# Kernel tuning notes

Hardware: AMD Instinct MI355X
Metric: run time of the kernel (lower is better)

Reference implementation:

```python
import jax, jax.numpy as jnp
import numpy as np

NB_CLUSTERS = 128   # C: number of clusters (equal-size, sorted ids)
PTS_PER_CLUSTER = 1024  # P: points per cluster
DIM = 3


def setup_inputs() -> dict:
    key = jax.random.key(0)
    k1, k2 = jax.random.split(key)
    n = NB_CLUSTERS * PTS_PER_CLUSTER
    input_points = jax.random.normal(k1, (n, DIM), dtype=jnp.float32)
    output_points = jax.random.normal(k2, (n, DIM), dtype=jnp.float32)
    clusters = jnp.repeat(jnp.arange(NB_CLUSTERS, dtype=jnp.int32), PTS_PER_CLUSTER)
    return {
        "input_points": input_points,
        "input_clusters": clusters,
        "output_points": output_points,
        "output_clusters": clusters,
    }


def reference(input_points, input_clusters, output_points, output_clusters):
    # Original: nb_clusters = max(input_clusters); loop for i in range(nb_clusters)
    # -> the HIGHEST cluster id is excluded from the loss. Reproduced via mask.
    nb = jnp.max(input_clusters)  # == NB_CLUSTERS - 1
    a = input_points.reshape(NB_CLUSTERS, PTS_PER_CLUSTER, DIM)   # [C,P,3]
    b = output_points.reshape(NB_CLUSTERS, PTS_PER_CLUSTER, DIM)  # [C,P,3]

    # Pairwise squared distances per cluster: d[c,i,j] = ||a[c,i]-b[c,j]||^2
    d = (jnp.sum(a * a, axis=-1)[:, :, None]
         + jnp.sum(b * b, axis=-1)[:, None, :]
         - 2.0 * jnp.einsum('cid,cjd->cij', a, b))  # [C,P,P]

    # Indices computed under no_grad in the original (ints: no grad anyway).
    idx1 = jnp.argmin(d, axis=2)  # for each input point: nearest output point
    idx2 = jnp.argmin(d, axis=1)  # for each output point: nearest input point

    near_b = jnp.take_along_axis(b, idx1[..., None], axis=1)  # [C,P,3]
    near_a = jnp.take_along_axis(a, idx2[..., None], axis=1)  # [C,P,3]

    l1 = jnp.sum((a - near_b) ** 2, axis=(1, 2))  # [C]
    l2 = jnp.sum((b - near_a) ** 2, axis=(1, 2))  # [C]

    mask = (jnp.arange(NB_CLUSTERS) < nb).astype(a.dtype)  # exclude last cluster
    return jnp.sum(mask * (l1 + l2))
```

## Files before the change

### kernel.cpp

```cpp
#include <hip/hip_runtime.h>


#define PTS  1024
#define ACTIVE_CLUSTERS 127
#define QG   64
#define Q    16
#define SEG  16
#define TPB  1024
#define TSEG (PTS / SEG)

typedef float v2f __attribute__((ext_vector_type(2)));

static __device__ __forceinline__ v2f splat2(float a) {
    v2f r; r.x = a; r.y = a; return r;
}

__global__
__attribute__((amdgpu_flat_work_group_size(TPB, TPB), amdgpu_waves_per_eu(4, 4)))
void chamfer_kernel(
    const float* __restrict__ pts_in,
    const float* __restrict__ pts_out,
    float* __restrict__ out)
{
    const int c   = blockIdx.x >> 1;
    const int dir = blockIdx.x & 1;

    const float* __restrict__ query  = dir ? pts_out : pts_in;
    const float* __restrict__ target = dir ? pts_in  : pts_out;

    __shared__ __align__(16) float sx[PTS];
    __shared__ __align__(16) float sy[PTS];
    __shared__ __align__(16) float sz[PTS];
    __shared__ __align__(16) float sh[PTS];
    __shared__ unsigned colmin[PTS];
    __shared__ float wsum[16];

    const int tid = threadIdx.x;
    const int qi  = tid & (QG - 1);
    const int seg = tid >> 6;
    const size_t base = (size_t)c * PTS * 3;

    colmin[tid] = 0x7f7fffffu;

    {
        const float* tp = target + base + (size_t)tid * 3;
        float x = tp[0], y = tp[1], z = tp[2];
        sx[tid] = x; sy[tid] = y; sz[tid] = z;
        sh[tid] = fmaf(x, x, fmaf(y, y, z * z));
    }

    float qx[Q], qy[Q], qz[Q], mn[Q];
    #pragma unroll
    for (int k = 0; k < Q; ++k) {
        const float* qp = query + base + (size_t)(k * QG + qi) * 3;
        qx[k] = -2.0f * qp[0];
        qy[k] = -2.0f * qp[1];
        qz[k] = -2.0f * qp[2];
        mn[k] = 3.4e38f;
    }
    __syncthreads();

    const int j0 = seg * TSEG;
    #pragma unroll 1
    for (int jj = 0; jj < TSEG; jj += 4) {
        const float4 bx = *(const float4*)&sx[j0 + jj];
        const float4 by = *(const float4*)&sy[j0 + jj];
        const float4 bz = *(const float4*)&sz[j0 + jj];
        const float4 bh = *(const float4*)&sh[j0 + jj];
        v2f bx01; bx01.x = bx.x; bx01.y = bx.y;
        v2f bx23; bx23.x = bx.z; bx23.y = bx.w;
        v2f by01; by01.x = by.x; by01.y = by.y;
        v2f by23; by23.x = by.z; by23.y = by.w;
        v2f bz01; bz01.x = bz.x; bz01.y = bz.y;
        v2f bz23; bz23.x = bz.z; bz23.y = bz.w;
        v2f bh01; bh01.x = bh.x; bh01.y = bh.y;
        v2f bh23; bh23.x = bh.z; bh23.y = bh.w;
        #pragma unroll
        for (int k = 0; k < Q; ++k) {
            v2f s01 = __builtin_elementwise_fma(splat2(qx[k]), bx01, bh01);
            s01 = __builtin_elementwise_fma(splat2(qy[k]), by01, s01);
            s01 = __builtin_elementwise_fma(splat2(qz[k]), bz01, s01);
            v2f s23 = __builtin_elementwise_fma(splat2(qx[k]), bx23, bh23);
            s23 = __builtin_elementwise_fma(splat2(qy[k]), by23, s23);
            s23 = __builtin_elementwise_fma(splat2(qz[k]), bz23, s23);
            mn[k] = fminf(fminf(s01.x, s01.y), mn[k]);
            mn[k] = fminf(fminf(s23.x, s23.y), mn[k]);
        }
    }

    #pragma unroll
    for (int k = 0; k < Q; ++k) {
        float n2 = fmaf(qx[k], qx[k], fmaf(qy[k], qy[k], qz[k] * qz[k]));
        float v  = fmaf(0.25f, n2, mn[k]);
        atomicMin(&colmin[k * QG + qi], __float_as_uint(v));
    }
    __syncthreads();

    float v = __uint_as_float(colmin[tid]);
    #pragma unroll
    for (int off = 32; off > 0; off >>= 1)
        v += __shfl_down(v, off, 64);

    const int wave = tid >> 6;
    const int lane = tid & 63;
    if (lane == 0) wsum[wave] = v;
    __syncthreads();

    if (wave == 0) {
        float t = (lane < 16) ? wsum[lane] : 0.0f;
        #pragma unroll
        for (int off = 8; off > 0; off >>= 1)
            t += __shfl_down(t, off, 64);
        if (lane == 0) atomicAdd(out, t);
    }
}

extern "C" void kernel_launch(void* const* d_in, const int* in_sizes, int n_in,
                              void* d_out, int out_size, void* d_ws, size_t ws_size,
                              hipStream_t stream) {
    const float* input_points  = (const float*)d_in[0];
    const float* output_points = (const float*)d_in[2];
    float* out = (float*)d_out;

    hipMemsetAsync(out, 0, sizeof(float), stream);

    chamfer_kernel<<<dim3(ACTIVE_CLUSTERS * 2), dim3(TPB), 0, stream>>>(
        input_points, output_points, out);
}
```

Before: 87.74 us.

## Split each cluster-direction block into two query halves and drop packed FMA

Each (cluster, direction) pair is now handled by two blocks, each owning half of the 1024 query points (8 per thread instead of 16). This doubles the grid so the 256 CUs get about two blocks each, giving more resident waves to hide latency. The packed v2f FMA inner loop is replaced with scalar fmaf chains, and the explicit waves-per-EU attribute is swapped for launch_bounds. The trade-offs are that every block reloads the full target set into LDS and issues more partial atomicAdds, and scalar FMAs may lose the dual-issue throughput of packed FP32 math.

```diff
diff --git a/kernel.cpp b/kernel.cpp
--- a/kernel.cpp
+++ b/kernel.cpp
@@ -1,29 +1,24 @@
 #include <hip/hip_runtime.h>
 
 
-#define PTS  1024
+#define PTS   1024
 #define ACTIVE_CLUSTERS 127
-#define QG   64
-#define Q    16
-#define SEG  16
-#define TPB  1024
-#define TSEG (PTS / SEG)
+#define QHALF 512
+#define QG    64
+#define Q     8
+#define SEG   16
+#define TPB   1024
+#define TSEG  (PTS / SEG)
 
-typedef float v2f __attribute__((ext_vector_type(2)));
-
-static __device__ __forceinline__ v2f splat2(float a) {
-    v2f r; r.x = a; r.y = a; return r;
-}
-
-__global__
-__attribute__((amdgpu_flat_work_group_size(TPB, TPB), amdgpu_waves_per_eu(4, 4)))
-void chamfer_kernel(
+__global__ __launch_bounds__(TPB) void chamfer_kernel(
     const float* __restrict__ pts_in,
     const float* __restrict__ pts_out,
     float* __restrict__ out)
 {
-    const int c   = blockIdx.x >> 1;
-    const int dir = blockIdx.x & 1;
+    const int b    = blockIdx.x;
+    const int c    = b >> 2;
+    const int dir  = (b >> 1) & 1;
+    const int half = b & 1;
 
     const float* __restrict__ query  = dir ? pts_out : pts_in;
     const float* __restrict__ target = dir ? pts_in  : pts_out;
@@ -32,7 +27,7 @@
     __shared__ __align__(16) float sy[PTS];
     __shared__ __align__(16) float sz[PTS];
     __shared__ __align__(16) float sh[PTS];
-    __shared__ unsigned colmin[PTS];
+    __shared__ unsigned colmin[QHALF];
     __shared__ float wsum[16];
 
     const int tid = threadIdx.x;
@@ -40,7 +35,7 @@
     const int seg = tid >> 6;
     const size_t base = (size_t)c * PTS * 3;
 
-    colmin[tid] = 0x7f7fffffu;
+    if (tid < QHALF) colmin[tid] = 0x7f7fffffu;
 
     {
         const float* tp = target + base + (size_t)tid * 3;
@@ -52,7 +47,8 @@
     float qx[Q], qy[Q], qz[Q], mn[Q];
     #pragma unroll
     for (int k = 0; k < Q; ++k) {
-        const float* qp = query + base + (size_t)(k * QG + qi) * 3;
+        const float* qp = query + base
+                        + (size_t)(half * QHALF + k * QG + qi) * 3;
         qx[k] = -2.0f * qp[0];
         qy[k] = -2.0f * qp[1];
         qz[k] = -2.0f * qp[2];
@@ -67,24 +63,14 @@
         const float4 by = *(const float4*)&sy[j0 + jj];
         const float4 bz = *(const float4*)&sz[j0 + jj];
         const float4 bh = *(const float4*)&sh[j0 + jj];
-        v2f bx01; bx01.x = bx.x; bx01.y = bx.y;
-        v2f bx23; bx23.x = bx.z; bx23.y = bx.w;
-        v2f by01; by01.x = by.x; by01.y = by.y;
-        v2f by23; by23.x = by.z; by23.y = by.w;
-        v2f bz01; bz01.x = bz.x; bz01.y = bz.y;
-        v2f bz23; bz23.x = bz.z; bz23.y = bz.w;
-        v2f bh01; bh01.x = bh.x; bh01.y = bh.y;
-        v2f bh23; bh23.x = bh.z; bh23.y = bh.w;
         #pragma unroll
         for (int k = 0; k < Q; ++k) {
-            v2f s01 = __builtin_elementwise_fma(splat2(qx[k]), bx01, bh01);
-            s01 = __builtin_elementwise_fma(splat2(qy[k]), by01, s01);
-            s01 = __builtin_elementwise_fma(splat2(qz[k]), bz01, s01);
-            v2f s23 = __builtin_elementwise_fma(splat2(qx[k]), bx23, bh23);
-            s23 = __builtin_elementwise_fma(splat2(qy[k]), by23, s23);
-            s23 = __builtin_elementwise_fma(splat2(qz[k]), bz23, s23);
-            mn[k] = fminf(fminf(s01.x, s01.y), mn[k]);
-            mn[k] = fminf(fminf(s23.x, s23.y), mn[k]);
+            float s0 = fmaf(qx[k], bx.x, fmaf(qy[k], by.x, fmaf(qz[k], bz.x, bh.x)));
+            float s1 = fmaf(qx[k], bx.y, fmaf(qy[k], by.y, fmaf(qz[k], bz.y, bh.y)));
+            float s2 = fmaf(qx[k], bx.z, fmaf(qy[k], by.z, fmaf(qz[k], bz.z, bh.z)));
+            float s3 = fmaf(qx[k], bx.w, fmaf(qy[k], by.w, fmaf(qz[k], bz.w, bh.w)));
+            mn[k] = fminf(fminf(s0, s1), mn[k]);
+            mn[k] = fminf(fminf(s2, s3), mn[k]);
         }
     }
 
@@ -96,7 +82,7 @@
     }
     __syncthreads();
 
-    float v = __uint_as_float(colmin[tid]);
+    float v = (tid < QHALF) ? __uint_as_float(colmin[tid]) : 0.0f;
     #pragma unroll
     for (int off = 32; off > 0; off >>= 1)
         v += __shfl_down(v, off, 64);
@@ -124,6 +110,6 @@
 
     hipMemsetAsync(out, 0, sizeof(float), stream);
 
-    chamfer_kernel<<<dim3(ACTIVE_CLUSTERS * 2), dim3(TPB), 0, stream>>>(
+    chamfer_kernel<<<dim3(ACTIVE_CLUSTERS * 2 * 2), dim3(TPB), 0, stream>>>(
         input_points, output_points, out);
 }
```

Measured after the change: 87.17 us. Within noise of the previous version (-0.7%).
